# Optimization experiments

Measured on AMD Instinct MI355X. Metric: run time of the kernel, lower is better.

## Reference

```python
import jax, jax.numpy as jnp
import numpy as np

N = 200_000   # mesh nodes
C = 400_000   # cells (~2N for triangular mesh)
K = 3 * C     # cells_node / cells_index flat length (3 nodes per cell)
E = 600_000   # cell-cell edges (faces)
D = 128       # feature dim
H = 128       # MLP hidden


def setup_inputs() -> dict:
    key = jax.random.key(0)
    ks = jax.random.split(key, 6)
    node_attr = jax.random.normal(ks[0], (N, D), dtype=jnp.float32)
    edge_attr = jax.random.normal(ks[1], (E, D), dtype=jnp.float32)
    W1 = jax.random.normal(ks[2], (3 * D, H), dtype=jnp.float32) * 0.05
    b1 = jnp.zeros((H,), dtype=jnp.float32)
    W2 = jax.random.normal(ks[3], (H, D), dtype=jnp.float32) * 0.05
    b2 = jnp.zeros((D,), dtype=jnp.float32)
    cells_node = jax.random.randint(ks[4], (K,), 0, N, dtype=jnp.int32)
    # each cell owns 3 consecutive node slots (faithful FVM incidence structure)
    cells_index = jnp.repeat(jnp.arange(C, dtype=jnp.int32), 3)
    edge_index = jax.random.randint(ks[5], (2, E), 0, C, dtype=jnp.int32)
    return dict(node_attr=node_attr, edge_attr=edge_attr, W1=W1, b1=b1,
                W2=W2, b2=b2, cells_node=cells_node, cells_index=cells_index,
                edge_index=edge_index)


def reference(node_attr, edge_attr, W1, b1, W2, b2,
              cells_node, cells_index, edge_index):
    # node -> cell scatter-sum (calc_cell_centered_with_node_attr, map=True)
    gathered = node_attr[cells_node]                      # [K, D]
    cell_attr = jax.ops.segment_sum(gathered, cells_index, num_segments=C)  # [C, D]
    senders, receivers = edge_index[0], edge_index[1]
    mask = (senders != receivers)[:, None].astype(node_attr.dtype)  # [E, 1]
    senders_attr = cell_attr[senders]                     # [E, D]
    receivers_attr = cell_attr[receivers] * mask          # zero self-edges
    collected = jnp.concatenate([senders_attr, receivers_attr, edge_attr], axis=1)  # [E, 3D]
    h = jax.nn.relu(collected @ W1 + b1)                  # [E, H]
    edge_attr_new = h @ W2 + b2                           # [E, D]
    return edge_attr_new
```

## Files before the change

kernel.cpp:

```cpp
#include <hip/hip_runtime.h>

typedef short bf16x8 __attribute__((ext_vector_type(8)));
typedef float f32x4 __attribute__((ext_vector_type(4)));

#define MAX_C 400000

__device__ __align__(16) unsigned short g_W1t[128 * 384];
__device__ __align__(16) unsigned short g_W2t[128 * 128];
__device__ __align__(16) unsigned short g_cell[((size_t)MAX_C + 1) * 128];

__device__ __forceinline__ unsigned short f2bf(float f) {
    union { unsigned int i; float f; } v; v.f = f;
    return (unsigned short)((v.i + 0x7FFFu + ((v.i >> 16) & 1u)) >> 16);
}

__global__ __launch_bounds__(256) void cell_kernel(
        const float* __restrict__ node_attr,
        const int* __restrict__ cells_node, int C)
{
    int t = threadIdx.x;
    int grp = blockIdx.x * 16 + (t >> 4);
    int sub = t & 15;
    int c0 = grp * 2, c1 = c0 + 1;
    if (c0 >= C) return;
    bool d1 = (c1 < C);

    int ja[3], jb[3];
    ja[0] = cells_node[c0 * 3 + 0];
    ja[1] = cells_node[c0 * 3 + 1];
    ja[2] = cells_node[c0 * 3 + 2];
    jb[0] = d1 ? cells_node[c1 * 3 + 0] : ja[0];
    jb[1] = d1 ? cells_node[c1 * 3 + 1] : ja[1];
    jb[2] = d1 ? cells_node[c1 * 3 + 2] : ja[2];

    float aL[4] = {0.f,0.f,0.f,0.f}, aH[4] = {0.f,0.f,0.f,0.f};
    float bL[4] = {0.f,0.f,0.f,0.f}, bH[4] = {0.f,0.f,0.f,0.f};
    #pragma unroll
    for (int j = 0; j < 3; ++j) {
        const float* r = node_attr + (size_t)ja[j] * 128;
        float4 lo = *(const float4*)(r + sub * 4);
        float4 hi = *(const float4*)(r + 64 + sub * 4);
        aL[0] += lo.x; aL[1] += lo.y; aL[2] += lo.z; aL[3] += lo.w;
        aH[0] += hi.x; aH[1] += hi.y; aH[2] += hi.z; aH[3] += hi.w;
    }
    #pragma unroll
    for (int j = 0; j < 3; ++j) {
        const float* r = node_attr + (size_t)jb[j] * 128;
        float4 lo = *(const float4*)(r + sub * 4);
        float4 hi = *(const float4*)(r + 64 + sub * 4);
        bL[0] += lo.x; bL[1] += lo.y; bL[2] += lo.z; bL[3] += lo.w;
        bH[0] += hi.x; bH[1] += hi.y; bH[2] += hi.z; bH[3] += hi.w;
    }
    uint2 o;
    o.x = (unsigned)f2bf(aL[0]) | ((unsigned)f2bf(aL[1]) << 16);
    o.y = (unsigned)f2bf(aL[2]) | ((unsigned)f2bf(aL[3]) << 16);
    *(uint2*)(g_cell + (size_t)c0 * 128 + sub * 4) = o;
    o.x = (unsigned)f2bf(aH[0]) | ((unsigned)f2bf(aH[1]) << 16);
    o.y = (unsigned)f2bf(aH[2]) | ((unsigned)f2bf(aH[3]) << 16);
    *(uint2*)(g_cell + (size_t)c0 * 128 + 64 + sub * 4) = o;
    if (d1) {
        o.x = (unsigned)f2bf(bL[0]) | ((unsigned)f2bf(bL[1]) << 16);
        o.y = (unsigned)f2bf(bL[2]) | ((unsigned)f2bf(bL[3]) << 16);
        *(uint2*)(g_cell + (size_t)c1 * 128 + sub * 4) = o;
        o.x = (unsigned)f2bf(bH[0]) | ((unsigned)f2bf(bH[1]) << 16);
        o.y = (unsigned)f2bf(bH[2]) | ((unsigned)f2bf(bH[3]) << 16);
        *(uint2*)(g_cell + (size_t)c1 * 128 + 64 + sub * 4) = o;
    }
}

__global__ __launch_bounds__(256) void wprep_kernel(
        const float* __restrict__ W1,
        const float* __restrict__ W2)
{
    int i = blockIdx.x * 256 + threadIdx.x;
    if (i < 384 * 128) {
        int n = i / 384, k = i % 384;
        g_W1t[i] = f2bf(W1[k * 128 + n]);
    } else {
        int j = i - 384 * 128;
        int n = j / 128, k = j % 128;
        g_W2t[j] = f2bf(W2[k * 128 + n]);
    }
}

__global__ __launch_bounds__(256) void edge_mlp_kernel(
        const float* __restrict__ edge_attr,
        const float* __restrict__ b1,
        const float* __restrict__ b2,
        const int* __restrict__ senders,
        const int* __restrict__ receivers,
        float* __restrict__ out, int E)
{
    __shared__ __align__(16) unsigned short Hs[128][136];

    const int t  = threadIdx.x;
    const int wv = t >> 6;
    const int l  = t & 63;
    const int lr = l & 15;
    const int q  = l >> 4;
    const int e0 = blockIdx.x * 128;
    const int eb = e0 + wv * 32;

    unsigned os[2], orr[2]; int eidx[2];
    #pragma unroll
    for (int nt = 0; nt < 2; ++nt) {
        int e = eb + nt * 16 + lr;
        if (e > E - 1) e = E - 1;
        eidx[nt] = e;
        int s = senders[e];
        int r = receivers[e];
        os[nt]  = (unsigned)s * 256u;
        orr[nt] = (s == r) ? (unsigned)MAX_C * 256u : (unsigned)r * 256u;
    }

    const char* cellb = (const char*)g_cell;
    const char* w1b   = (const char*)g_W1t;
    const char* w2b   = (const char*)g_W2t;
    const unsigned qb = (unsigned)(q * 16);

    f32x4 acc[8][2];
    #pragma unroll
    for (int mt = 0; mt < 8; ++mt) { acc[mt][0] = (f32x4)(0.f); acc[mt][1] = (f32x4)(0.f); }

    bf16x8 bB[3][2];
    float4 rL[3][2], rH[3][2];

    auto loadB = [&](int kc) {
        int p = kc % 3;
        if (kc < 4) {
            #pragma unroll
            for (int nt = 0; nt < 2; ++nt)
                bB[p][nt] = *(const bf16x8*)(cellb + (size_t)(os[nt] + qb + kc * 64));
        } else if (kc < 8) {
            #pragma unroll
            for (int nt = 0; nt < 2; ++nt)
                bB[p][nt] = *(const bf16x8*)(cellb + (size_t)(orr[nt] + qb + (kc - 4) * 64));
        } else {
            #pragma unroll
            for (int nt = 0; nt < 2; ++nt) {
                const float* pp = edge_attr + (size_t)eidx[nt] * 128 + (kc - 8) * 32 + q * 8;
                rL[p][nt] = *(const float4*)(pp);
                rH[p][nt] = *(const float4*)(pp + 4);
            }
        }
    };
    auto getB = [&](int kc, int nt) -> bf16x8 {
        int p = kc % 3;
        if (kc < 8) return bB[p][nt];
        union { unsigned short u[8]; bf16x8 v; } r;
        float4 lo = rL[p][nt], hi = rH[p][nt];
        r.u[0] = f2bf(lo.x); r.u[1] = f2bf(lo.y); r.u[2] = f2bf(lo.z); r.u[3] = f2bf(lo.w);
        r.u[4] = f2bf(hi.x); r.u[5] = f2bf(hi.y); r.u[6] = f2bf(hi.z); r.u[7] = f2bf(hi.w);
        return r.v;
    };

    loadB(0); loadB(1);
    #pragma unroll
    for (int kc = 0; kc < 12; ++kc) {
        if (kc + 2 < 12) loadB(kc + 2);
        bf16x8 bb0 = getB(kc, 0);
        bf16x8 bb1 = getB(kc, 1);
        #pragma unroll
        for (int mt = 0; mt < 8; ++mt) {
            bf16x8 a = *(const bf16x8*)(w1b + (size_t)((mt * 16 + lr) * 768 + kc * 64 + qb));
            acc[mt][0] = __builtin_amdgcn_mfma_f32_16x16x32_bf16(a, bb0, acc[mt][0], 0, 0, 0);
            acc[mt][1] = __builtin_amdgcn_mfma_f32_16x16x32_bf16(a, bb1, acc[mt][1], 0, 0, 0);
        }
    }

    #pragma unroll
    for (int mt = 0; mt < 8; ++mt) {
        const int f = mt * 16 + q * 4;
        const float4 bv = *(const float4*)(b1 + f);
        #pragma unroll
        for (int nt = 0; nt < 2; ++nt) {
            int el = wv * 32 + nt * 16 + lr;
            float v0 = acc[mt][nt][0] + bv.x; v0 = v0 > 0.f ? v0 : 0.f;
            float v1 = acc[mt][nt][1] + bv.y; v1 = v1 > 0.f ? v1 : 0.f;
            float v2 = acc[mt][nt][2] + bv.z; v2 = v2 > 0.f ? v2 : 0.f;
            float v3 = acc[mt][nt][3] + bv.w; v3 = v3 > 0.f ? v3 : 0.f;
            uint2 w;
            w.x = (unsigned)f2bf(v0) | ((unsigned)f2bf(v1) << 16);
            w.y = (unsigned)f2bf(v2) | ((unsigned)f2bf(v3) << 16);
            *(uint2*)&Hs[el][f] = w;
        }
    }

    f32x4 acc2[8][2];
    #pragma unroll
    for (int mt = 0; mt < 8; ++mt) { acc2[mt][0] = (f32x4)(0.f); acc2[mt][1] = (f32x4)(0.f); }

    #pragma unroll
    for (int kc = 0; kc < 4; ++kc) {
        bf16x8 h0 = *(const bf16x8*)&Hs[wv * 32 +      lr][kc * 32 + q * 8];
        bf16x8 h1 = *(const bf16x8*)&Hs[wv * 32 + 16 + lr][kc * 32 + q * 8];
        #pragma unroll
        for (int mt = 0; mt < 8; ++mt) {
            bf16x8 a = *(const bf16x8*)(w2b + (size_t)((mt * 16 + lr) * 256 + kc * 64 + qb));
            acc2[mt][0] = __builtin_amdgcn_mfma_f32_16x16x32_bf16(a, h0, acc2[mt][0], 0, 0, 0);
            acc2[mt][1] = __builtin_amdgcn_mfma_f32_16x16x32_bf16(a, h1, acc2[mt][1], 0, 0, 0);
        }
    }

    #pragma unroll
    for (int mt = 0; mt < 8; ++mt) {
        const int f = mt * 16 + q * 4;
        const float4 bv = *(const float4*)(b2 + f);
        #pragma unroll
        for (int nt = 0; nt < 2; ++nt) {
            int e = eb + nt * 16 + lr;
            if (e < E) {
                float4 v;
                v.x = acc2[mt][nt][0] + bv.x;
                v.y = acc2[mt][nt][1] + bv.y;
                v.z = acc2[mt][nt][2] + bv.z;
                v.w = acc2[mt][nt][3] + bv.w;
                *(float4*)(out + (size_t)e * 128 + f) = v;
            }
        }
    }
}

extern "C" void kernel_launch(void* const* d_in, const int* in_sizes, int n_in,
                              void* d_out, int out_size, void* d_ws, size_t ws_size,
                              hipStream_t stream)
{
    const float* node_attr = (const float*)d_in[0];
    const float* edge_attr = (const float*)d_in[1];
    const float* W1 = (const float*)d_in[2];
    const float* b1 = (const float*)d_in[3];
    const float* W2 = (const float*)d_in[4];
    const float* b2 = (const float*)d_in[5];
    const int* cells_node  = (const int*)d_in[6];
    const int* edge_index  = (const int*)d_in[8];
    float* out = (float*)d_out;

    int E = in_sizes[1] / 128;
    int C = in_sizes[6] / 3;

    const int* senders = edge_index;
    const int* receivers = edge_index + E;

    hipLaunchKernelGGL(cell_kernel, dim3((C + 31) / 32), dim3(256), 0, stream,
                       node_attr, cells_node, C);
    hipLaunchKernelGGL(wprep_kernel, dim3(256), dim3(256), 0, stream, W1, W2);
    hipLaunchKernelGGL(edge_mlp_kernel, dim3((E + 127) / 128), dim3(256), 0, stream,
                       edge_attr, b1, b2, senders, receivers, out, E);
}
```

Before: 1.004 ms.

## Prefetch all gathered cell rows upfront and software-pipeline W1 loads with sched barriers

The edge MLP kernel now issues every sender and receiver cell-row gather at the start, plus half the edge_attr loads. It then double-buffers the W1 fragments in registers across k-chunks, with sched_barrier to force each load to overlap the MFMAs of the previous chunk. The cell kernel is restructured so 4 threads handle one cell with 32 floats each, issuing all 24 vector loads before summing and writing 16-byte stores. Launch bounds request 2 blocks per CU; the much higher register count from holding many prefetched fragments may cost occupancy or cause spills.

New measurement: 1.016 ms. No clear change (+1.2%).

```diff
diff --git a/kernel.cpp b/kernel.cpp
--- a/kernel.cpp
+++ b/kernel.cpp
@@ -4,6 +4,7 @@
 typedef float f32x4 __attribute__((ext_vector_type(4)));
 
 #define MAX_C 400000
+#define SBAR() __builtin_amdgcn_sched_barrier(0)
 
 __device__ __align__(16) unsigned short g_W1t[128 * 384];
 __device__ __align__(16) unsigned short g_W2t[128 * 128];
@@ -19,52 +20,44 @@
         const int* __restrict__ cells_node, int C)
 {
     int t = threadIdx.x;
-    int grp = blockIdx.x * 16 + (t >> 4);
-    int sub = t & 15;
-    int c0 = grp * 2, c1 = c0 + 1;
-    if (c0 >= C) return;
-    bool d1 = (c1 < C);
-
-    int ja[3], jb[3];
-    ja[0] = cells_node[c0 * 3 + 0];
-    ja[1] = cells_node[c0 * 3 + 1];
-    ja[2] = cells_node[c0 * 3 + 2];
-    jb[0] = d1 ? cells_node[c1 * 3 + 0] : ja[0];
-    jb[1] = d1 ? cells_node[c1 * 3 + 1] : ja[1];
-    jb[2] = d1 ? cells_node[c1 * 3 + 2] : ja[2];
-
-    float aL[4] = {0.f,0.f,0.f,0.f}, aH[4] = {0.f,0.f,0.f,0.f};
-    float bL[4] = {0.f,0.f,0.f,0.f}, bH[4] = {0.f,0.f,0.f,0.f};
-    #pragma unroll
-    for (int j = 0; j < 3; ++j) {
-        const float* r = node_attr + (size_t)ja[j] * 128;
-        float4 lo = *(const float4*)(r + sub * 4);
-        float4 hi = *(const float4*)(r + 64 + sub * 4);
-        aL[0] += lo.x; aL[1] += lo.y; aL[2] += lo.z; aL[3] += lo.w;
-        aH[0] += hi.x; aH[1] += hi.y; aH[2] += hi.z; aH[3] += hi.w;
-    }
-    #pragma unroll
-    for (int j = 0; j < 3; ++j) {
-        const float* r = node_attr + (size_t)jb[j] * 128;
-        float4 lo = *(const float4*)(r + sub * 4);
-        float4 hi = *(const float4*)(r + 64 + sub * 4);
-        bL[0] += lo.x; bL[1] += lo.y; bL[2] += lo.z; bL[3] += lo.w;
-        bH[0] += hi.x; bH[1] += hi.y; bH[2] += hi.z; bH[3] += hi.w;
-    }
-    uint2 o;
-    o.x = (unsigned)f2bf(aL[0]) | ((unsigned)f2bf(aL[1]) << 16);
-    o.y = (unsigned)f2bf(aL[2]) | ((unsigned)f2bf(aL[3]) << 16);
-    *(uint2*)(g_cell + (size_t)c0 * 128 + sub * 4) = o;
-    o.x = (unsigned)f2bf(aH[0]) | ((unsigned)f2bf(aH[1]) << 16);
-    o.y = (unsigned)f2bf(aH[2]) | ((unsigned)f2bf(aH[3]) << 16);
-    *(uint2*)(g_cell + (size_t)c0 * 128 + 64 + sub * 4) = o;
-    if (d1) {
-        o.x = (unsigned)f2bf(bL[0]) | ((unsigned)f2bf(bL[1]) << 16);
-        o.y = (unsigned)f2bf(bL[2]) | ((unsigned)f2bf(bL[3]) << 16);
-        *(uint2*)(g_cell + (size_t)c1 * 128 + sub * 4) = o;
-        o.x = (unsigned)f2bf(bH[0]) | ((unsigned)f2bf(bH[1]) << 16);
-        o.y = (unsigned)f2bf(bH[2]) | ((unsigned)f2bf(bH[3]) << 16);
-        *(uint2*)(g_cell + (size_t)c1 * 128 + 64 + sub * 4) = o;
+    int cell = blockIdx.x * 64 + (t >> 2);
+    int sub = t & 3;
+    if (cell >= C) return;
+    int j0 = cells_node[cell * 3 + 0];
+    int j1 = cells_node[cell * 3 + 1];
+    int j2 = cells_node[cell * 3 + 2];
+    const float* r0 = node_attr + (size_t)j0 * 128 + sub * 32;
+    const float* r1 = node_attr + (size_t)j1 * 128 + sub * 32;
+    const float* r2 = node_attr + (size_t)j2 * 128 + sub * 32;
+
+    float4 v0[8], v1[8], v2[8];
+    #pragma unroll
+    for (int i = 0; i < 8; ++i) v0[i] = *(const float4*)(r0 + i * 4);
+    #pragma unroll
+    for (int i = 0; i < 8; ++i) v1[i] = *(const float4*)(r1 + i * 4);
+    #pragma unroll
+    for (int i = 0; i < 8; ++i) v2[i] = *(const float4*)(r2 + i * 4);
+    SBAR();
+
+    unsigned short* dst = g_cell + (size_t)cell * 256 / 2 * 2;
+    dst = g_cell + (size_t)cell * 128 + sub * 32;
+    #pragma unroll
+    for (int h = 0; h < 4; ++h) {
+        float4 sA, sB;
+        sA.x = v0[2*h].x + v1[2*h].x + v2[2*h].x;
+        sA.y = v0[2*h].y + v1[2*h].y + v2[2*h].y;
+        sA.z = v0[2*h].z + v1[2*h].z + v2[2*h].z;
+        sA.w = v0[2*h].w + v1[2*h].w + v2[2*h].w;
+        sB.x = v0[2*h+1].x + v1[2*h+1].x + v2[2*h+1].x;
+        sB.y = v0[2*h+1].y + v1[2*h+1].y + v2[2*h+1].y;
+        sB.z = v0[2*h+1].z + v1[2*h+1].z + v2[2*h+1].z;
+        sB.w = v0[2*h+1].w + v1[2*h+1].w + v2[2*h+1].w;
+        uint4 o;
+        o.x = (unsigned)f2bf(sA.x) | ((unsigned)f2bf(sA.y) << 16);
+        o.y = (unsigned)f2bf(sA.z) | ((unsigned)f2bf(sA.w) << 16);
+        o.z = (unsigned)f2bf(sB.x) | ((unsigned)f2bf(sB.y) << 16);
+        o.w = (unsigned)f2bf(sB.z) | ((unsigned)f2bf(sB.w) << 16);
+        *(uint4*)(dst + h * 8) = o;
     }
 }
 
@@ -83,7 +76,7 @@
     }
 }
 
-__global__ __launch_bounds__(256) void edge_mlp_kernel(
+__global__ __launch_bounds__(256, 2) void edge_mlp_kernel(
         const float* __restrict__ edge_attr,
         const float* __restrict__ b1,
         const float* __restrict__ b2,
@@ -101,72 +94,89 @@
     const int e0 = blockIdx.x * 128;
     const int eb = e0 + wv * 32;
 
-    unsigned os[2], orr[2]; int eidx[2];
-    #pragma unroll
-    for (int nt = 0; nt < 2; ++nt) {
-        int e = eb + nt * 16 + lr;
-        if (e > E - 1) e = E - 1;
-        eidx[nt] = e;
-        int s = senders[e];
-        int r = receivers[e];
-        os[nt]  = (unsigned)s * 256u;
-        orr[nt] = (s == r) ? (unsigned)MAX_C * 256u : (unsigned)r * 256u;
-    }
+    const int ei0 = min(eb + lr,      E - 1);
+    const int ei1 = min(eb + 16 + lr, E - 1);
+    const int s0 = senders[ei0], r0i = receivers[ei0];
+    const int s1 = senders[ei1], r1i = receivers[ei1];
+
+    const unsigned qb = (unsigned)(q * 16);
+    const unsigned so0 = (unsigned)s0 * 256u + qb;
+    const unsigned so1 = (unsigned)s1 * 256u + qb;
+    const unsigned ro0 = ((s0 == r0i) ? (unsigned)MAX_C * 256u : (unsigned)r0i * 256u) + qb;
+    const unsigned ro1 = ((s1 == r1i) ? (unsigned)MAX_C * 256u : (unsigned)r1i * 256u) + qb;
 
     const char* cellb = (const char*)g_cell;
     const char* w1b   = (const char*)g_W1t;
     const char* w2b   = (const char*)g_W2t;
-    const unsigned qb = (unsigned)(q * 16);
+    const float* ep0 = edge_attr + (size_t)ei0 * 128 + q * 8;
+    const float* ep1 = edge_attr + (size_t)ei1 * 128 + q * 8;
 
     f32x4 acc[8][2];
     #pragma unroll
     for (int mt = 0; mt < 8; ++mt) { acc[mt][0] = (f32x4)(0.f); acc[mt][1] = (f32x4)(0.f); }
 
-    bf16x8 bB[3][2];
-    float4 rL[3][2], rH[3][2];
-
-    auto loadB = [&](int kc) {
-        int p = kc % 3;
-        if (kc < 4) {
-            #pragma unroll
-            for (int nt = 0; nt < 2; ++nt)
-                bB[p][nt] = *(const bf16x8*)(cellb + (size_t)(os[nt] + qb + kc * 64));
-        } else if (kc < 8) {
-            #pragma unroll
-            for (int nt = 0; nt < 2; ++nt)
-                bB[p][nt] = *(const bf16x8*)(cellb + (size_t)(orr[nt] + qb + (kc - 4) * 64));
-        } else {
-            #pragma unroll
-            for (int nt = 0; nt < 2; ++nt) {
-                const float* pp = edge_attr + (size_t)eidx[nt] * 128 + (kc - 8) * 32 + q * 8;
-                rL[p][nt] = *(const float4*)(pp);
-                rH[p][nt] = *(const float4*)(pp + 4);
-            }
-        }
+    bf16x8 sF0[4], sF1[4], rF0[4], rF1[4];
+    float4 eL0[4], eH0[4], eL1[4], eH1[4];
+    #pragma unroll
+    for (int c = 0; c < 4; ++c) {
+        sF0[c] = *(const bf16x8*)(cellb + (size_t)(so0 + c * 64));
+        sF1[c] = *(const bf16x8*)(cellb + (size_t)(so1 + c * 64));
+    }
+    #pragma unroll
+    for (int c = 0; c < 4; ++c) {
+        rF0[c] = *(const bf16x8*)(cellb + (size_t)(ro0 + c * 64));
+        rF1[c] = *(const bf16x8*)(cellb + (size_t)(ro1 + c * 64));
+    }
+
+    bf16x8 aA[8], aB[8];
+    auto loadA1 = [&](bf16x8 (&aD)[8], int kc) {
+        #pragma unroll
+        for (int mt = 0; mt < 8; ++mt)
+            aD[mt] = *(const bf16x8*)(w1b + (size_t)((mt * 16 + lr) * 768 + kc * 64 + qb));
     };
-    auto getB = [&](int kc, int nt) -> bf16x8 {
-        int p = kc % 3;
-        if (kc < 8) return bB[p][nt];
+    auto step = [&](bf16x8 bb0, bf16x8 bb1, bf16x8 (&aC)[8]) {
+        #pragma unroll
+        for (int mt = 0; mt < 8; ++mt) {
+            acc[mt][0] = __builtin_amdgcn_mfma_f32_16x16x32_bf16(aC[mt], bb0, acc[mt][0], 0, 0, 0);
+            acc[mt][1] = __builtin_amdgcn_mfma_f32_16x16x32_bf16(aC[mt], bb1, acc[mt][1], 0, 0, 0);
+        }
+    };
+    auto cvt = [&](float4 lo, float4 hi) -> bf16x8 {
         union { unsigned short u[8]; bf16x8 v; } r;
-        float4 lo = rL[p][nt], hi = rH[p][nt];
         r.u[0] = f2bf(lo.x); r.u[1] = f2bf(lo.y); r.u[2] = f2bf(lo.z); r.u[3] = f2bf(lo.w);
         r.u[4] = f2bf(hi.x); r.u[5] = f2bf(hi.y); r.u[6] = f2bf(hi.z); r.u[7] = f2bf(hi.w);
         return r.v;
     };
 
-    loadB(0); loadB(1);
-    #pragma unroll
-    for (int kc = 0; kc < 12; ++kc) {
-        if (kc + 2 < 12) loadB(kc + 2);
-        bf16x8 bb0 = getB(kc, 0);
-        bf16x8 bb1 = getB(kc, 1);
-        #pragma unroll
-        for (int mt = 0; mt < 8; ++mt) {
-            bf16x8 a = *(const bf16x8*)(w1b + (size_t)((mt * 16 + lr) * 768 + kc * 64 + qb));
-            acc[mt][0] = __builtin_amdgcn_mfma_f32_16x16x32_bf16(a, bb0, acc[mt][0], 0, 0, 0);
-            acc[mt][1] = __builtin_amdgcn_mfma_f32_16x16x32_bf16(a, bb1, acc[mt][1], 0, 0, 0);
-        }
-    }
+    loadA1(aA, 0);
+    #pragma unroll
+    for (int c = 0; c < 2; ++c) {
+        eL0[c] = *(const float4*)(ep0 + c * 32);
+        eH0[c] = *(const float4*)(ep0 + c * 32 + 4);
+        eL1[c] = *(const float4*)(ep1 + c * 32);
+        eH1[c] = *(const float4*)(ep1 + c * 32 + 4);
+    }
+    SBAR();
+    loadA1(aB, 1);  step(sF0[0], sF1[0], aA);  SBAR();
+    loadA1(aA, 2);  step(sF0[1], sF1[1], aB);  SBAR();
+    loadA1(aB, 3);  step(sF0[2], sF1[2], aA);  SBAR();
+    loadA1(aA, 4);  step(sF0[3], sF1[3], aB);  SBAR();
+    loadA1(aB, 5);
+    #pragma unroll
+    for (int c = 2; c < 4; ++c) {
+        eL0[c] = *(const float4*)(ep0 + c * 32);
+        eH0[c] = *(const float4*)(ep0 + c * 32 + 4);
+        eL1[c] = *(const float4*)(ep1 + c * 32);
+        eH1[c] = *(const float4*)(ep1 + c * 32 + 4);
+    }
+    step(rF0[0], rF1[0], aA);  SBAR();
+    loadA1(aA, 6);  step(rF0[1], rF1[1], aB);  SBAR();
+    loadA1(aB, 7);  step(rF0[2], rF1[2], aA);  SBAR();
+    loadA1(aA, 8);  step(rF0[3], rF1[3], aB);  SBAR();
+    loadA1(aB, 9);  step(cvt(eL0[0], eH0[0]), cvt(eL1[0], eH1[0]), aA);  SBAR();
+    loadA1(aA, 10); step(cvt(eL0[1], eH0[1]), cvt(eL1[1], eH1[1]), aB);  SBAR();
+    loadA1(aB, 11); step(cvt(eL0[2], eH0[2]), cvt(eL1[2], eH1[2]), aA);  SBAR();
+    step(cvt(eL0[3], eH0[3]), cvt(eL1[3], eH1[3]), aB);
 
     #pragma unroll
     for (int mt = 0; mt < 8; ++mt) {
@@ -174,7 +184,6 @@
         const float4 bv = *(const float4*)(b1 + f);
         #pragma unroll
         for (int nt = 0; nt < 2; ++nt) {
-            int el = wv * 32 + nt * 16 + lr;
             float v0 = acc[mt][nt][0] + bv.x; v0 = v0 > 0.f ? v0 : 0.f;
             float v1 = acc[mt][nt][1] + bv.y; v1 = v1 > 0.f ? v1 : 0.f;
             float v2 = acc[mt][nt][2] + bv.z; v2 = v2 > 0.f ? v2 : 0.f;
@@ -182,7 +191,7 @@
             uint2 w;
             w.x = (unsigned)f2bf(v0) | ((unsigned)f2bf(v1) << 16);
             w.y = (unsigned)f2bf(v2) | ((unsigned)f2bf(v3) << 16);
-            *(uint2*)&Hs[el][f] = w;
+            *(uint2*)&Hs[wv * 32 + nt * 16 + lr][f] = w;
         }
     }
 
@@ -200,6 +209,7 @@
             acc2[mt][0] = __builtin_amdgcn_mfma_f32_16x16x32_bf16(a, h0, acc2[mt][0], 0, 0, 0);
             acc2[mt][1] = __builtin_amdgcn_mfma_f32_16x16x32_bf16(a, h1, acc2[mt][1], 0, 0, 0);
         }
+        SBAR();
     }
 
     #pragma unroll
@@ -241,7 +251,7 @@
     const int* senders = edge_index;
     const int* receivers = edge_index + E;
 
-    hipLaunchKernelGGL(cell_kernel, dim3((C + 31) / 32), dim3(256), 0, stream,
+    hipLaunchKernelGGL(cell_kernel, dim3((C + 63) / 64), dim3(256), 0, stream,
                        node_attr, cells_node, C);
     hipLaunchKernelGGL(wprep_kernel, dim3(256), dim3(256), 0, stream, W1, W2);
     hipLaunchKernelGGL(edge_mlp_kernel, dim3((E + 127) / 128), dim3(256), 0, stream,
```
